# Kernel tuning notes

Measured on AMD Instinct MI355X. Metric: run time of the kernel, lower is better.

Reference implementation:

```python
import jax, jax.numpy as jnp
import numpy as np

NUM_HEAD = 8
HEAD_DIM = 64
MAX_LEN = 2048
FEAT_DIM = 512
BATCH = 2
TEMPERATURE = 10000.0


def positional_encoding(L, F, temperature=TEMPERATURE):
    # Faithful port of get_positional_encoding (torch.range is inclusive -> L / F elements)
    embed = jnp.arange(L, dtype=jnp.float32)
    dim_t = jnp.arange(F, dtype=jnp.float32)
    dim_t = temperature ** (2.0 * jnp.floor(dim_t / 2.0) / F)
    pos = embed[:, None] / dim_t                      # (L, F)
    pos = jnp.stack([jnp.sin(pos[:, 0::2]), jnp.cos(pos[:, 1::2])], axis=2)  # (L, F//2, 2)
    return pos.reshape(1, L, F)


def setup_inputs() -> dict:
    key = jax.random.key(0)
    ks = jax.random.split(key, 7)
    D = NUM_HEAD * HEAD_DIM
    scale = 1.0 / np.sqrt(FEAT_DIM)
    return {
        "inputs": jax.random.normal(ks[0], (BATCH, FEAT_DIM, MAX_LEN), dtype=jnp.float32),
        "Wq": jax.random.normal(ks[1], (D, FEAT_DIM), dtype=jnp.float32) * scale,
        "bq": jax.random.normal(ks[2], (D,), dtype=jnp.float32) * 0.01,
        "Wk": jax.random.normal(ks[3], (D, FEAT_DIM), dtype=jnp.float32) * scale,
        "bk": jax.random.normal(ks[4], (D,), dtype=jnp.float32) * 0.01,
        "Wv": jax.random.normal(ks[5], (D, FEAT_DIM), dtype=jnp.float32) * scale,
        "bv": jax.random.normal(ks[6], (D,), dtype=jnp.float32) * 0.01,
    }


def reference(inputs, Wq, bq, Wk, bk, Wv, bv):
    B, F, L = inputs.shape
    H, d = NUM_HEAD, HEAD_DIM
    pos = positional_encoding(L, F)                   # (1, L, F)
    x = jnp.transpose(inputs, (0, 2, 1))              # (B, L, F)
    qk_in = x + pos
    q = (qk_in @ Wq.T + bq).reshape(B, L, H, d)       # (B, L, H, d)
    k = (qk_in @ Wk.T + bk).reshape(B, L, H, d)
    v = x @ Wv.T + bv                                 # computed but unused (bug in original)
    del v
    # NOTE: original uses KEY heads as values (multi_head_value built from key)
    scores = jnp.einsum("bqhd,bkhd->bhqk", q, k) * (float(d) ** -0.5)
    attn = jax.nn.softmax(scores, axis=-1)            # (B, H, L, L)
    dist = jnp.einsum("bhqk,bkhd->bqhd", attn, k).reshape(B, L, H * d)
    attn_out = jnp.transpose(attn, (0, 2, 3, 1))      # (B, L, L, H) == cat of head splits on -1
    return dist, attn_out
```

## Files before the change

kernel.cpp:

```cpp
#include <hip/hip_runtime.h>
#include <math.h>

constexpr int LSEQ = 2048;
constexpr int FEAT = 512;
constexpr int NH = 8;
constexpr int DM = 512;
constexpr int NB = 2;

typedef __bf16 bf16x8 __attribute__((ext_vector_type(8)));
typedef unsigned short u16x8 __attribute__((ext_vector_type(8)));
typedef unsigned int u32x4 __attribute__((ext_vector_type(4)));
typedef float f32x4 __attribute__((ext_vector_type(4)));

#define EXPC 0.18033688011112042f

__device__ inline f32x4 mfma16(u16x8 a, u16x8 b, f32x4 c) {
  return __builtin_amdgcn_mfma_f32_16x16x32_bf16(
      __builtin_bit_cast(bf16x8, a), __builtin_bit_cast(bf16x8, b), c, 0, 0, 0);
}
__device__ inline unsigned cvtpk(float lo, float hi) {
  unsigned r;
  asm("v_cvt_pk_bf16_f32 %0, %1, %2" : "=v"(r) : "v"(lo), "v"(hi));
  return r;
}
__device__ inline u16x8 ldbf8(const unsigned short* p) {
  return *reinterpret_cast<const u16x8*>(p);
}

__global__ __launch_bounds__(256) void pos_kernel(float* __restrict__ posT) {
  int idx = blockIdx.x * 256 + threadIdx.x;
  int l = idx & (LSEQ - 1);
  int f = idx >> 11;
  int i = f >> 1;
  double t = exp((double)i * (9.210340371976184 / 256.0));
  float ang = (float)((double)l / t);
  posT[idx] = (f & 1) ? cosf(ang) : sinf(ang);
}

__global__ __launch_bounds__(256) void prep_kernel(const float* __restrict__ x,
                                                   const float* __restrict__ posT,
                                                   unsigned short* __restrict__ abuf) {
  __shared__ float As[64 * 68];
  const int t = threadIdx.x;
  const int bid = blockIdx.x;
  const int ft = bid & 7, lt = (bid >> 3) & 31, b = bid >> 8;
  const int f0 = ft * 64, l0 = lt * 64;
#pragma unroll
  for (int rep = 0; rep < 4; ++rep) {
    int fl = rep * 16 + (t >> 4), l4 = (t & 15) * 4;
    float4 xv = *(const float4*)(x + ((size_t)b * FEAT + f0 + fl) * LSEQ + l0 + l4);
    float4 pv = *(const float4*)(posT + (size_t)(f0 + fl) * LSEQ + l0 + l4);
    *(float4*)&As[fl * 68 + l4] = make_float4(xv.x + pv.x, xv.y + pv.y, xv.z + pv.z, xv.w + pv.w);
  }
  __syncthreads();
  const int ll = t >> 2, fc = t & 3;
#pragma unroll
  for (int rep = 0; rep < 4; ++rep) {
    int fb = (fc + rep * 4) * 4;
    float v0 = As[(fb + 0) * 68 + ll];
    float v1 = As[(fb + 1) * 68 + ll];
    float v2 = As[(fb + 2) * 68 + ll];
    float v3 = As[(fb + 3) * 68 + ll];
    uint2 u = make_uint2(cvtpk(v0, v1), cvtpk(v2, v3));
    *(uint2*)(abuf + ((size_t)(b * LSEQ + l0 + ll)) * 512 + f0 + fb) = u;
  }
}

__global__ __launch_bounds__(256) void wcvt_kernel(const float* __restrict__ Wq,
                                                   const float* __restrict__ Wk,
                                                   unsigned short* __restrict__ wbuf) {
  int i8 = blockIdx.x * 256 + threadIdx.x;
  size_t base = (size_t)i8 * 8;
  const float* src = (base < (size_t)512 * 512) ? Wq + base : Wk + (base - (size_t)512 * 512);
  float4 a = *(const float4*)src;
  float4 b4 = *(const float4*)(src + 4);
  *(uint2*)(wbuf + base) = make_uint2(cvtpk(a.x, a.y), cvtpk(a.z, a.w));
  *(uint2*)(wbuf + base + 4) = make_uint2(cvtpk(b4.x, b4.y), cvtpk(b4.z, b4.w));
}

__global__ __launch_bounds__(256) void proj_kernel(
    const unsigned short* __restrict__ abuf, const unsigned short* __restrict__ wbuf,
    const float* __restrict__ bq, const float* __restrict__ bk,
    unsigned short* __restrict__ qb, unsigned short* __restrict__ kb,
    unsigned short* __restrict__ kT) {
  const int t = threadIdx.x;
  const int c0 = blockIdx.x * 64;
  const int r0 = blockIdx.y * 64;
  const int w = t >> 6, l = t & 63;
  const int lr = l & 15, g = l >> 4;
  const int c0w = c0 + (w >> 1) * 32;
  const int r0w = r0 + (w & 1) * 32;
  f32x4 acc[2][2];
#pragma unroll
  for (int i = 0; i < 2; ++i)
#pragma unroll
    for (int j = 0; j < 2; ++j) acc[i][j] = (f32x4){0.f, 0.f, 0.f, 0.f};
  for (int f0 = 0; f0 < FEAT; f0 += 32) {
    u16x8 a0 = ldbf8(wbuf + (size_t)(c0w + lr) * 512 + f0 + g * 8);
    u16x8 a1 = ldbf8(wbuf + (size_t)(c0w + 16 + lr) * 512 + f0 + g * 8);
    u16x8 b0 = ldbf8(abuf + (size_t)(r0w + lr) * 512 + f0 + g * 8);
    u16x8 b1 = ldbf8(abuf + (size_t)(r0w + 16 + lr) * 512 + f0 + g * 8);
    acc[0][0] = mfma16(a0, b0, acc[0][0]);
    acc[0][1] = mfma16(a0, b1, acc[0][1]);
    acc[1][0] = mfma16(a1, b0, acc[1][0]);
    acc[1][1] = mfma16(a1, b1, acc[1][1]);
  }
  const int isK = (c0 >= DM);
  const float* bias = isK ? bk : bq;
  unsigned short* ob = isK ? kb : qb;
  const int cb = c0w & (DM - 1);
#pragma unroll
  for (int ch = 0; ch < 2; ++ch) {
    int c = cb + ch * 16 + g * 4;
    float b0v = bias[c], b1v = bias[c + 1], b2v = bias[c + 2], b3v = bias[c + 3];
#pragma unroll
    for (int rh = 0; rh < 2; ++rh) {
      int r = r0w + rh * 16 + lr;
      f32x4 v = acc[ch][rh];
      uint2 u = make_uint2(cvtpk(v[0] + b0v, v[1] + b1v), cvtpk(v[2] + b2v, v[3] + b3v));
      *(uint2*)(ob + (size_t)r * 512 + c) = u;
      if (isK) {
        int bsel = r >> 11, lq = r & (LSEQ - 1);
        unsigned short* kp = kT + ((size_t)(bsel * 512 + c)) * 2048 + lq;
        kp[0] = (unsigned short)(u.x & 0xffff);
        kp[2048] = (unsigned short)(u.x >> 16);
        kp[2 * 2048] = (unsigned short)(u.y & 0xffff);
        kp[3 * 2048] = (unsigned short)(u.y >> 16);
      }
    }
  }
}

__global__ __launch_bounds__(512) void pass1_kernel(
    const unsigned short* __restrict__ qb, const unsigned short* __restrict__ kb,
    float* __restrict__ lpart) {
  const int t = threadIdx.x;
  const int bid = blockIdx.x;
  const int sp = bid & 7, qt = (bid >> 3) & 31, b = bid >> 8;
  const int q0 = qt * 64;
  const int h = t >> 6, l = t & 63;
  const int lr = l & 15, g = l >> 4;
  u16x8 qf[4][2];
#pragma unroll
  for (int Mt = 0; Mt < 4; ++Mt)
#pragma unroll
    for (int dh = 0; dh < 2; ++dh)
      qf[Mt][dh] = ldbf8(qb + (size_t)(b * LSEQ + q0 + Mt * 16 + lr) * 512 + h * 64 + dh * 32 + g * 8);
  float sum[4] = {0.f, 0.f, 0.f, 0.f};
  for (int slab = 0; slab < 8; ++slab) {
    const int kk0 = sp * 256 + slab * 32;
    u16x8 af[2][2];
#pragma unroll
    for (int kh = 0; kh < 2; ++kh)
#pragma unroll
      for (int dh = 0; dh < 2; ++dh)
        af[kh][dh] = ldbf8(kb + (size_t)(b * LSEQ + kk0 + kh * 16 + lr) * 512 + h * 64 + dh * 32 + g * 8);
#pragma unroll
    for (int Mt = 0; Mt < 4; ++Mt)
#pragma unroll
      for (int kh = 0; kh < 2; ++kh) {
        f32x4 s = (f32x4){0.f, 0.f, 0.f, 0.f};
        s = mfma16(af[kh][0], qf[Mt][0], s);
        s = mfma16(af[kh][1], qf[Mt][1], s);
        sum[Mt] += exp2f(s[0] * EXPC) + exp2f(s[1] * EXPC) +
                   exp2f(s[2] * EXPC) + exp2f(s[3] * EXPC);
      }
  }
#pragma unroll
  for (int Mt = 0; Mt < 4; ++Mt) {
    float v = sum[Mt];
    v += __shfl_xor(v, 16);
    v += __shfl_xor(v, 32);
    if ((l & 48) == 0)
      lpart[((size_t)((b * 8 + sp) * LSEQ) + q0 + Mt * 16 + lr) * 8 + h] = v;
  }
}

__global__ __launch_bounds__(512) void pass2_kernel(
    const unsigned short* __restrict__ qb, const unsigned short* __restrict__ kb,
    const unsigned short* __restrict__ kT, const float* __restrict__ lpart,
    float* __restrict__ attn, float* __restrict__ dist, float* __restrict__ distp) {
  __shared__ float Ps[2 * 32 * 292];
  __shared__ float linv[256];
  const int t = threadIdx.x;
  const int bid = blockIdx.x;
  const int qt = bid & 63;
  const int sp = (bid >> 6) & 1;
  const int b = bid >> 7;
  const int q0 = qt * 32;
  if (t < 256) {
    int q = t >> 3, hh = t & 7;
    float s = 0.f;
#pragma unroll
    for (int p = 0; p < 8; ++p)
      s += lpart[((size_t)((b * 8 + p) * LSEQ) + q0 + q) * 8 + hh];
    linv[t] = 1.0f / s;
  }
  __syncthreads();
  const int h = t >> 6, l = t & 63;
  const int lr = l & 15, g = l >> 4;
  u16x8 qf[2][2];
#pragma unroll
  for (int Mt = 0; Mt < 2; ++Mt)
#pragma unroll
    for (int dh = 0; dh < 2; ++dh)
      qf[Mt][dh] = ldbf8(qb + (size_t)(b * LSEQ + q0 + Mt * 16 + lr) * 512 + h * 64 + dh * 32 + g * 8);
  float lv[2] = {linv[lr * 8 + h], linv[(16 + lr) * 8 + h]};
  f32x4 dacc[2][4];
#pragma unroll
  for (int Mt = 0; Mt < 2; ++Mt)
#pragma unroll
    for (int Nd = 0; Nd < 4; ++Nd) dacc[Mt][Nd] = (f32x4){0.f, 0.f, 0.f, 0.f};

  const int kkb = sp * 1024;
  for (int slab = 0; slab < 32; ++slab) {
    const int kk0 = kkb + slab * 32;
    float* Pc = &Ps[(slab & 1) * 9344];
    u16x8 af[2][2];
#pragma unroll
    for (int kh = 0; kh < 2; ++kh)
#pragma unroll
      for (int dh = 0; dh < 2; ++dh)
        af[kh][dh] = ldbf8(kb + (size_t)(b * LSEQ + kk0 + kh * 16 + lr) * 512 + h * 64 + dh * 32 + g * 8);
    u16x8 bt[4];
#pragma unroll
    for (int Nd = 0; Nd < 4; ++Nd)
      bt[Nd] = ldbf8(kT + (size_t)(b * 512 + h * 64 + Nd * 16 + lr) * 2048 + kk0 + g * 8);
#pragma unroll
    for (int Mt = 0; Mt < 2; ++Mt)
#pragma unroll
      for (int kh = 0; kh < 2; ++kh) {
        f32x4 s = (f32x4){0.f, 0.f, 0.f, 0.f};
        s = mfma16(af[kh][0], qf[Mt][0], s);
        s = mfma16(af[kh][1], qf[Mt][1], s);
        f32x4 e = {exp2f(s[0] * EXPC) * lv[Mt], exp2f(s[1] * EXPC) * lv[Mt],
                   exp2f(s[2] * EXPC) * lv[Mt], exp2f(s[3] * EXPC) * lv[Mt]};
        *(f32x4*)&Pc[(Mt * 16 + lr) * 292 + h * 36 + kh * 16 + g * 4] = e;
      }
    __syncthreads();
#pragma unroll
    for (int rep = 0; rep < 4; ++rep) {
      int F = rep * 512 + t;
      int q = F >> 6, kk = (F >> 1) & 31, hh = (F & 1) * 4;
      int pb = q * 292 + hh * 36 + kk;
      f32x4 v = {Pc[pb], Pc[pb + 36], Pc[pb + 72], Pc[pb + 108]};
      __builtin_nontemporal_store(v,
          (f32x4*)(attn + ((size_t)(b * LSEQ + q0 + q)) * (LSEQ * NH) + (size_t)(kk0 + kk) * 8 + hh));
    }
#pragma unroll
    for (int Mt = 0; Mt < 2; ++Mt) {
      int pb = (Mt * 16 + lr) * 292 + h * 36 + g * 8;
      f32x4 plo = *(const f32x4*)&Pc[pb];
      f32x4 phi = *(const f32x4*)&Pc[pb + 4];
      u32x4 pu = {cvtpk(plo[0], plo[1]), cvtpk(plo[2], plo[3]),
                  cvtpk(phi[0], phi[1]), cvtpk(phi[2], phi[3])};
      u16x8 pa = __builtin_bit_cast(u16x8, pu);
#pragma unroll
      for (int Nd = 0; Nd < 4; ++Nd)
        dacc[Mt][Nd] = mfma16(pa, bt[Nd], dacc[Mt][Nd]);
    }
  }
  float* dp = sp ? distp : dist;
#pragma unroll
  for (int Mt = 0; Mt < 2; ++Mt)
#pragma unroll
    for (int Nd = 0; Nd < 4; ++Nd)
#pragma unroll
      for (int r = 0; r < 4; ++r)
        dp[((size_t)(b * LSEQ + q0 + Mt * 16 + g * 4 + r)) * 512 + h * 64 + Nd * 16 + lr] =
            dacc[Mt][Nd][r];
}

__global__ __launch_bounds__(256) void combine_kernel(const float* __restrict__ p,
                                                      float* __restrict__ dist) {
  int i4 = blockIdx.x * 256 + threadIdx.x;
  const float4* p4 = (const float4*)p;
  float4 a = ((float4*)dist)[i4], c = p4[i4];
  ((float4*)dist)[i4] = make_float4(a.x + c.x, a.y + c.y, a.z + c.z, a.w + c.w);
}

extern "C" void kernel_launch(void* const* d_in, const int* in_sizes, int n_in,
                              void* d_out, int out_size, void* d_ws, size_t ws_size,
                              hipStream_t stream) {
  const float* x  = (const float*)d_in[0];
  const float* Wq = (const float*)d_in[1];
  const float* bq = (const float*)d_in[2];
  const float* Wk = (const float*)d_in[3];
  const float* bk = (const float*)d_in[4];
  float* out  = (float*)d_out;
  float* dist = out;
  float* attn = out + (size_t)NB * LSEQ * DM;
  float* ws = (float*)d_ws;
  float* posT  = ws;
  unsigned short* abuf = (unsigned short*)(ws + 1048576);
  unsigned short* wbuf = (unsigned short*)(ws + 2097152);
  unsigned short* qb   = (unsigned short*)(ws + 2359296);
  unsigned short* kb   = (unsigned short*)(ws + 3407872);
  unsigned short* kT   = (unsigned short*)(ws + 4456448);
  float* lpart = ws + 5505024;
  float* distp = ws;

  pos_kernel<<<4096, 256, 0, stream>>>(posT);
  prep_kernel<<<512, 256, 0, stream>>>(x, posT, abuf);
  wcvt_kernel<<<256, 256, 0, stream>>>(Wq, Wk, wbuf);
  proj_kernel<<<dim3(16, 64), 256, 0, stream>>>(abuf, wbuf, bq, bk, qb, kb, kT);
  pass1_kernel<<<512, 512, 0, stream>>>(qb, kb, lpart);
  pass2_kernel<<<256, 512, 0, stream>>>(qb, kb, kT, lpart, attn, dist, distp);
  combine_kernel<<<2048, 256, 0, stream>>>(distp, dist);
}
```

Before: 171.1 us.

## Fuse softmax passes into one kernel, compute positional encoding inline, fold scale into Q

After: 223.6 us. +30.7%, slower.

```diff
diff --git a/kernel.cpp b/kernel.cpp
--- a/kernel.cpp
+++ b/kernel.cpp
@@ -13,6 +13,7 @@
 typedef float f32x4 __attribute__((ext_vector_type(4)));
 
 #define EXPC 0.18033688011112042f
+#define L2TEN4 13.287712379549449f
 
 __device__ inline f32x4 mfma16(u16x8 a, u16x8 b, f32x4 c) {
   return __builtin_amdgcn_mfma_f32_16x16x32_bf16(
@@ -26,31 +27,47 @@
 __device__ inline u16x8 ldbf8(const unsigned short* p) {
   return *reinterpret_cast<const u16x8*>(p);
 }
-
-__global__ __launch_bounds__(256) void pos_kernel(float* __restrict__ posT) {
-  int idx = blockIdx.x * 256 + threadIdx.x;
-  int l = idx & (LSEQ - 1);
-  int f = idx >> 11;
-  int i = f >> 1;
-  double t = exp((double)i * (9.210340371976184 / 256.0));
-  float ang = (float)((double)l / t);
-  posT[idx] = (f & 1) ? cosf(ang) : sinf(ang);
-}
-
-__global__ __launch_bounds__(256) void prep_kernel(const float* __restrict__ x,
-                                                   const float* __restrict__ posT,
-                                                   unsigned short* __restrict__ abuf) {
+__device__ inline f32x4 qk_chain(u16x8 a0, u16x8 a1, u16x8 q0, u16x8 q1) {
+  f32x4 s = (f32x4){0.f, 0.f, 0.f, 0.f};
+  s = mfma16(a0, q0, s);
+  s = mfma16(a1, q1, s);
+  return s;
+}
+
+__global__ __launch_bounds__(256) void prep_all_kernel(
+    const float* __restrict__ x, const float* __restrict__ Wq,
+    const float* __restrict__ Wk, unsigned short* __restrict__ abuf,
+    unsigned short* __restrict__ wbuf) {
+  const int t = threadIdx.x;
+  const int bid0 = blockIdx.x;
+  if (bid0 >= 512) {
+    int i8 = (bid0 - 512) * 256 + t;
+    size_t base = (size_t)i8 * 8;
+    const float* src = (base < (size_t)512 * 512) ? Wq + base : Wk + (base - (size_t)512 * 512);
+    float4 a = *(const float4*)src;
+    float4 b4 = *(const float4*)(src + 4);
+    *(uint2*)(wbuf + base) = make_uint2(cvtpk(a.x, a.y), cvtpk(a.z, a.w));
+    *(uint2*)(wbuf + base + 4) = make_uint2(cvtpk(b4.x, b4.y), cvtpk(b4.z, b4.w));
+    return;
+  }
   __shared__ float As[64 * 68];
-  const int t = threadIdx.x;
-  const int bid = blockIdx.x;
-  const int ft = bid & 7, lt = (bid >> 3) & 31, b = bid >> 8;
+  const int ft = bid0 & 7, lt = (bid0 >> 3) & 31, b = bid0 >> 8;
   const int f0 = ft * 64, l0 = lt * 64;
 #pragma unroll
   for (int rep = 0; rep < 4; ++rep) {
     int fl = rep * 16 + (t >> 4), l4 = (t & 15) * 4;
-    float4 xv = *(const float4*)(x + ((size_t)b * FEAT + f0 + fl) * LSEQ + l0 + l4);
-    float4 pv = *(const float4*)(posT + (size_t)(f0 + fl) * LSEQ + l0 + l4);
-    *(float4*)&As[fl * 68 + l4] = make_float4(xv.x + pv.x, xv.y + pv.y, xv.z + pv.z, xv.w + pv.w);
+    int f = f0 + fl;
+    float invt = exp2f((float)(f >> 1) * (-L2TEN4 / 256.0f));
+    float4 xv = *(const float4*)(x + ((size_t)b * FEAT + f) * LSEQ + l0 + l4);
+    float a0 = (float)(l0 + l4 + 0) * invt;
+    float a1 = (float)(l0 + l4 + 1) * invt;
+    float a2 = (float)(l0 + l4 + 2) * invt;
+    float a3 = (float)(l0 + l4 + 3) * invt;
+    float4 pv;
+    if (f & 1) { pv.x = cosf(a0); pv.y = cosf(a1); pv.z = cosf(a2); pv.w = cosf(a3); }
+    else       { pv.x = sinf(a0); pv.y = sinf(a1); pv.z = sinf(a2); pv.w = sinf(a3); }
+    *(float4*)&As[fl * 68 + l4] =
+        make_float4(xv.x + pv.x, xv.y + pv.y, xv.z + pv.z, xv.w + pv.w);
   }
   __syncthreads();
   const int ll = t >> 2, fc = t & 3;
@@ -61,21 +78,9 @@
     float v1 = As[(fb + 1) * 68 + ll];
     float v2 = As[(fb + 2) * 68 + ll];
     float v3 = As[(fb + 3) * 68 + ll];
-    uint2 u = make_uint2(cvtpk(v0, v1), cvtpk(v2, v3));
-    *(uint2*)(abuf + ((size_t)(b * LSEQ + l0 + ll)) * 512 + f0 + fb) = u;
-  }
-}
-
-__global__ __launch_bounds__(256) void wcvt_kernel(const float* __restrict__ Wq,
-                                                   const float* __restrict__ Wk,
-                                                   unsigned short* __restrict__ wbuf) {
-  int i8 = blockIdx.x * 256 + threadIdx.x;
-  size_t base = (size_t)i8 * 8;
-  const float* src = (base < (size_t)512 * 512) ? Wq + base : Wk + (base - (size_t)512 * 512);
-  float4 a = *(const float4*)src;
-  float4 b4 = *(const float4*)(src + 4);
-  *(uint2*)(wbuf + base) = make_uint2(cvtpk(a.x, a.y), cvtpk(a.z, a.w));
-  *(uint2*)(wbuf + base + 4) = make_uint2(cvtpk(b4.x, b4.y), cvtpk(b4.z, b4.w));
+    *(uint2*)(abuf + ((size_t)(b * LSEQ + l0 + ll)) * 512 + f0 + fb) =
+        make_uint2(cvtpk(v0, v1), cvtpk(v2, v3));
+  }
 }
 
 __global__ __launch_bounds__(256) void proj_kernel(
@@ -108,6 +113,7 @@
   const int isK = (c0 >= DM);
   const float* bias = isK ? bk : bq;
   unsigned short* ob = isK ? kb : qb;
+  const float scale = isK ? 1.0f : EXPC;
   const int cb = c0w & (DM - 1);
 #pragma unroll
   for (int ch = 0; ch < 2; ++ch) {
@@ -117,7 +123,8 @@
     for (int rh = 0; rh < 2; ++rh) {
       int r = r0w + rh * 16 + lr;
       f32x4 v = acc[ch][rh];
-      uint2 u = make_uint2(cvtpk(v[0] + b0v, v[1] + b1v), cvtpk(v[2] + b2v, v[3] + b3v));
+      uint2 u = make_uint2(cvtpk((v[0] + b0v) * scale, (v[1] + b1v) * scale),
+                           cvtpk((v[2] + b2v) * scale, (v[3] + b3v) * scale));
       *(uint2*)(ob + (size_t)r * 512 + c) = u;
       if (isK) {
         int bsel = r >> 11, lq = r & (LSEQ - 1);
@@ -131,115 +138,62 @@
   }
 }
 
-__global__ __launch_bounds__(512) void pass1_kernel(
+__global__ __launch_bounds__(512) void pass2_kernel(
     const unsigned short* __restrict__ qb, const unsigned short* __restrict__ kb,
-    float* __restrict__ lpart) {
+    const unsigned short* __restrict__ kT, float* __restrict__ attn,
+    float* __restrict__ dist) {
+  __shared__ float Ps[2 * 16 * 292];
   const int t = threadIdx.x;
   const int bid = blockIdx.x;
-  const int sp = bid & 7, qt = (bid >> 3) & 31, b = bid >> 8;
-  const int q0 = qt * 64;
+  const int qt = bid & 127;
+  const int b = bid >> 7;
+  const int q0 = qt * 16;
   const int h = t >> 6, l = t & 63;
   const int lr = l & 15, g = l >> 4;
-  u16x8 qf[4][2];
-#pragma unroll
-  for (int Mt = 0; Mt < 4; ++Mt)
-#pragma unroll
-    for (int dh = 0; dh < 2; ++dh)
-      qf[Mt][dh] = ldbf8(qb + (size_t)(b * LSEQ + q0 + Mt * 16 + lr) * 512 + h * 64 + dh * 32 + g * 8);
-  float sum[4] = {0.f, 0.f, 0.f, 0.f};
-  for (int slab = 0; slab < 8; ++slab) {
-    const int kk0 = sp * 256 + slab * 32;
-    u16x8 af[2][2];
-#pragma unroll
-    for (int kh = 0; kh < 2; ++kh)
-#pragma unroll
-      for (int dh = 0; dh < 2; ++dh)
-        af[kh][dh] = ldbf8(kb + (size_t)(b * LSEQ + kk0 + kh * 16 + lr) * 512 + h * 64 + dh * 32 + g * 8);
-#pragma unroll
-    for (int Mt = 0; Mt < 4; ++Mt)
-#pragma unroll
-      for (int kh = 0; kh < 2; ++kh) {
-        f32x4 s = (f32x4){0.f, 0.f, 0.f, 0.f};
-        s = mfma16(af[kh][0], qf[Mt][0], s);
-        s = mfma16(af[kh][1], qf[Mt][1], s);
-        sum[Mt] += exp2f(s[0] * EXPC) + exp2f(s[1] * EXPC) +
-                   exp2f(s[2] * EXPC) + exp2f(s[3] * EXPC);
-      }
-  }
-#pragma unroll
-  for (int Mt = 0; Mt < 4; ++Mt) {
-    float v = sum[Mt];
-    v += __shfl_xor(v, 16);
-    v += __shfl_xor(v, 32);
-    if ((l & 48) == 0)
-      lpart[((size_t)((b * 8 + sp) * LSEQ) + q0 + Mt * 16 + lr) * 8 + h] = v;
-  }
-}
-
-__global__ __launch_bounds__(512) void pass2_kernel(
-    const unsigned short* __restrict__ qb, const unsigned short* __restrict__ kb,
-    const unsigned short* __restrict__ kT, const float* __restrict__ lpart,
-    float* __restrict__ attn, float* __restrict__ dist, float* __restrict__ distp) {
-  __shared__ float Ps[2 * 32 * 292];
-  __shared__ float linv[256];
-  const int t = threadIdx.x;
-  const int bid = blockIdx.x;
-  const int qt = bid & 63;
-  const int sp = (bid >> 6) & 1;
-  const int b = bid >> 7;
-  const int q0 = qt * 32;
-  if (t < 256) {
-    int q = t >> 3, hh = t & 7;
-    float s = 0.f;
-#pragma unroll
-    for (int p = 0; p < 8; ++p)
-      s += lpart[((size_t)((b * 8 + p) * LSEQ) + q0 + q) * 8 + hh];
-    linv[t] = 1.0f / s;
-  }
-  __syncthreads();
-  const int h = t >> 6, l = t & 63;
-  const int lr = l & 15, g = l >> 4;
-  u16x8 qf[2][2];
-#pragma unroll
-  for (int Mt = 0; Mt < 2; ++Mt)
-#pragma unroll
-    for (int dh = 0; dh < 2; ++dh)
-      qf[Mt][dh] = ldbf8(qb + (size_t)(b * LSEQ + q0 + Mt * 16 + lr) * 512 + h * 64 + dh * 32 + g * 8);
-  float lv[2] = {linv[lr * 8 + h], linv[(16 + lr) * 8 + h]};
-  f32x4 dacc[2][4];
-#pragma unroll
-  for (int Mt = 0; Mt < 2; ++Mt)
-#pragma unroll
-    for (int Nd = 0; Nd < 4; ++Nd) dacc[Mt][Nd] = (f32x4){0.f, 0.f, 0.f, 0.f};
-
-  const int kkb = sp * 1024;
-  for (int slab = 0; slab < 32; ++slab) {
-    const int kk0 = kkb + slab * 32;
-    float* Pc = &Ps[(slab & 1) * 9344];
-    u16x8 af[2][2];
-#pragma unroll
-    for (int kh = 0; kh < 2; ++kh)
-#pragma unroll
-      for (int dh = 0; dh < 2; ++dh)
-        af[kh][dh] = ldbf8(kb + (size_t)(b * LSEQ + kk0 + kh * 16 + lr) * 512 + h * 64 + dh * 32 + g * 8);
+  u16x8 qf[2];
+#pragma unroll
+  for (int dh = 0; dh < 2; ++dh)
+    qf[dh] = ldbf8(qb + (size_t)(b * LSEQ + q0 + lr) * 512 + h * 64 + dh * 32 + g * 8);
+
+  float sum = 0.f;
+  for (int slab = 0; slab < 64; ++slab) {
+    const int kk0 = slab * 32;
+#pragma unroll
+    for (int kh = 0; kh < 2; ++kh) {
+      const unsigned short* kp = kb + (size_t)(b * LSEQ + kk0 + kh * 16 + lr) * 512 + h * 64 + g * 8;
+      u16x8 a0 = ldbf8(kp);
+      u16x8 a1 = ldbf8(kp + 32);
+      f32x4 s = qk_chain(a0, a1, qf[0], qf[1]);
+      sum += exp2f(s[0]) + exp2f(s[1]) + exp2f(s[2]) + exp2f(s[3]);
+    }
+  }
+  sum += __shfl_xor(sum, 16);
+  sum += __shfl_xor(sum, 32);
+  const float linv = 1.0f / sum;
+
+  f32x4 dacc[4];
+#pragma unroll
+  for (int Nd = 0; Nd < 4; ++Nd) dacc[Nd] = (f32x4){0.f, 0.f, 0.f, 0.f};
+  for (int slab = 0; slab < 64; ++slab) {
+    const int kk0 = slab * 32;
+    float* Pc = &Ps[(slab & 1) * 4672];
     u16x8 bt[4];
 #pragma unroll
     for (int Nd = 0; Nd < 4; ++Nd)
       bt[Nd] = ldbf8(kT + (size_t)(b * 512 + h * 64 + Nd * 16 + lr) * 2048 + kk0 + g * 8);
 #pragma unroll
-    for (int Mt = 0; Mt < 2; ++Mt)
-#pragma unroll
-      for (int kh = 0; kh < 2; ++kh) {
-        f32x4 s = (f32x4){0.f, 0.f, 0.f, 0.f};
-        s = mfma16(af[kh][0], qf[Mt][0], s);
-        s = mfma16(af[kh][1], qf[Mt][1], s);
-        f32x4 e = {exp2f(s[0] * EXPC) * lv[Mt], exp2f(s[1] * EXPC) * lv[Mt],
-                   exp2f(s[2] * EXPC) * lv[Mt], exp2f(s[3] * EXPC) * lv[Mt]};
-        *(f32x4*)&Pc[(Mt * 16 + lr) * 292 + h * 36 + kh * 16 + g * 4] = e;
-      }
+    for (int kh = 0; kh < 2; ++kh) {
+      const unsigned short* kp = kb + (size_t)(b * LSEQ + kk0 + kh * 16 + lr) * 512 + h * 64 + g * 8;
+      u16x8 a0 = ldbf8(kp);
+      u16x8 a1 = ldbf8(kp + 32);
+      f32x4 s = qk_chain(a0, a1, qf[0], qf[1]);
+      f32x4 e = {exp2f(s[0]) * linv, exp2f(s[1]) * linv,
+                 exp2f(s[2]) * linv, exp2f(s[3]) * linv};
+      *(f32x4*)&Pc[lr * 292 + h * 36 + kh * 16 + g * 4] = e;
+    }
     __syncthreads();
 #pragma unroll
-    for (int rep = 0; rep < 4; ++rep) {
+    for (int rep = 0; rep < 2; ++rep) {
       int F = rep * 512 + t;
       int q = F >> 6, kk = (F >> 1) & 31, hh = (F & 1) * 4;
       int pb = q * 292 + hh * 36 + kk;
@@ -247,9 +201,8 @@
       __builtin_nontemporal_store(v,
           (f32x4*)(attn + ((size_t)(b * LSEQ + q0 + q)) * (LSEQ * NH) + (size_t)(kk0 + kk) * 8 + hh));
     }
-#pragma unroll
-    for (int Mt = 0; Mt < 2; ++Mt) {
-      int pb = (Mt * 16 + lr) * 292 + h * 36 + g * 8;
+    {
+      int pb = lr * 292 + h * 36 + g * 8;
       f32x4 plo = *(const f32x4*)&Pc[pb];
       f32x4 phi = *(const f32x4*)&Pc[pb + 4];
       u32x4 pu = {cvtpk(plo[0], plo[1]), cvtpk(plo[2], plo[3]),
@@ -257,26 +210,14 @@
       u16x8 pa = __builtin_bit_cast(u16x8, pu);
 #pragma unroll
       for (int Nd = 0; Nd < 4; ++Nd)
-        dacc[Mt][Nd] = mfma16(pa, bt[Nd], dacc[Mt][Nd]);
-    }
-  }
-  float* dp = sp ? distp : dist;
-#pragma unroll
-  for (int Mt = 0; Mt < 2; ++Mt)
-#pragma unroll
-    for (int Nd = 0; Nd < 4; ++Nd)
-#pragma unroll
-      for (int r = 0; r < 4; ++r)
-        dp[((size_t)(b * LSEQ + q0 + Mt * 16 + g * 4 + r)) * 512 + h * 64 + Nd * 16 + lr] =
-            dacc[Mt][Nd][r];
-}
-
-__global__ __launch_bounds__(256) void combine_kernel(const float* __restrict__ p,
-                                                      float* __restrict__ dist) {
-  int i4 = blockIdx.x * 256 + threadIdx.x;
-  const float4* p4 = (const float4*)p;
-  float4 a = ((float4*)dist)[i4], c = p4[i4];
-  ((float4*)dist)[i4] = make_float4(a.x + c.x, a.y + c.y, a.z + c.z, a.w + c.w);
+        dacc[Nd] = mfma16(pa, bt[Nd], dacc[Nd]);
+    }
+  }
+#pragma unroll
+  for (int Nd = 0; Nd < 4; ++Nd)
+#pragma unroll
+    for (int r = 0; r < 4; ++r)
+      dist[((size_t)(b * LSEQ + q0 + g * 4 + r)) * 512 + h * 64 + Nd * 16 + lr] = dacc[Nd][r];
 }
 
 extern "C" void kernel_launch(void* const* d_in, const int* in_sizes, int n_in,
@@ -291,20 +232,13 @@
   float* dist = out;
   float* attn = out + (size_t)NB * LSEQ * DM;
   float* ws = (float*)d_ws;
-  float* posT  = ws;
-  unsigned short* abuf = (unsigned short*)(ws + 1048576);
-  unsigned short* wbuf = (unsigned short*)(ws + 2097152);
-  unsigned short* qb   = (unsigned short*)(ws + 2359296);
-  unsigned short* kb   = (unsigned short*)(ws + 3407872);
-  unsigned short* kT   = (unsigned short*)(ws + 4456448);
-  float* lpart = ws + 5505024;
-  float* distp = ws;
-
-  pos_kernel<<<4096, 256, 0, stream>>>(posT);
-  prep_kernel<<<512, 256, 0, stream>>>(x, posT, abuf);
-  wcvt_kernel<<<256, 256, 0, stream>>>(Wq, Wk, wbuf);
+  unsigned short* abuf = (unsigned short*)(ws);
+  unsigned short* wbuf = (unsigned short*)(ws + 1048576);
+  unsigned short* qb   = (unsigned short*)(ws + 1310720);
+  unsigned short* kb   = (unsigned short*)(ws + 2359296);
+  unsigned short* kT   = (unsigned short*)(ws + 3407872);
+
+  prep_all_kernel<<<768, 256, 0, stream>>>(x, Wq, Wk, abuf, wbuf);
   proj_kernel<<<dim3(16, 64), 256, 0, stream>>>(abuf, wbuf, bq, bk, qb, kb, kT);
-  pass1_kernel<<<512, 512, 0, stream>>>(qb, kb, lpart);
-  pass2_kernel<<<256, 512, 0, stream>>>(qb, kb, kT, lpart, attn, dist, distp);
-  combine_kernel<<<2048, 256, 0, stream>>>(distp, dist);
-}
+  pass2_kernel<<<256, 512, 0, stream>>>(qb, kb, kT, attn, dist);
+}
```

## Fuse positional encoding and weight conversion into one prep kernel, prescale Q

Applied to the files above, without the earlier changes.

Measured after the change: 162.1 us. -5.3%, faster.

```diff
diff --git a/kernel.cpp b/kernel.cpp
--- a/kernel.cpp
+++ b/kernel.cpp
@@ -13,6 +13,7 @@
 typedef float f32x4 __attribute__((ext_vector_type(4)));
 
 #define EXPC 0.18033688011112042f
+#define L2TEN4 13.287712379549449f
 
 __device__ inline f32x4 mfma16(u16x8 a, u16x8 b, f32x4 c) {
   return __builtin_amdgcn_mfma_f32_16x16x32_bf16(
@@ -26,31 +27,47 @@
 __device__ inline u16x8 ldbf8(const unsigned short* p) {
   return *reinterpret_cast<const u16x8*>(p);
 }
-
-__global__ __launch_bounds__(256) void pos_kernel(float* __restrict__ posT) {
-  int idx = blockIdx.x * 256 + threadIdx.x;
-  int l = idx & (LSEQ - 1);
-  int f = idx >> 11;
-  int i = f >> 1;
-  double t = exp((double)i * (9.210340371976184 / 256.0));
-  float ang = (float)((double)l / t);
-  posT[idx] = (f & 1) ? cosf(ang) : sinf(ang);
-}
-
-__global__ __launch_bounds__(256) void prep_kernel(const float* __restrict__ x,
-                                                   const float* __restrict__ posT,
-                                                   unsigned short* __restrict__ abuf) {
+__device__ inline f32x4 qk_chain(u16x8 a0, u16x8 a1, u16x8 q0, u16x8 q1) {
+  f32x4 s = (f32x4){0.f, 0.f, 0.f, 0.f};
+  s = mfma16(a0, q0, s);
+  s = mfma16(a1, q1, s);
+  return s;
+}
+
+__global__ __launch_bounds__(256) void prep_all_kernel(
+    const float* __restrict__ x, const float* __restrict__ Wq,
+    const float* __restrict__ Wk, unsigned short* __restrict__ abuf,
+    unsigned short* __restrict__ wbuf) {
+  const int t = threadIdx.x;
+  const int bid0 = blockIdx.x;
+  if (bid0 >= 512) {
+    int i8 = (bid0 - 512) * 256 + t;
+    size_t base = (size_t)i8 * 8;
+    const float* src = (base < (size_t)512 * 512) ? Wq + base : Wk + (base - (size_t)512 * 512);
+    float4 a = *(const float4*)src;
+    float4 b4 = *(const float4*)(src + 4);
+    *(uint2*)(wbuf + base) = make_uint2(cvtpk(a.x, a.y), cvtpk(a.z, a.w));
+    *(uint2*)(wbuf + base + 4) = make_uint2(cvtpk(b4.x, b4.y), cvtpk(b4.z, b4.w));
+    return;
+  }
   __shared__ float As[64 * 68];
-  const int t = threadIdx.x;
-  const int bid = blockIdx.x;
-  const int ft = bid & 7, lt = (bid >> 3) & 31, b = bid >> 8;
+  const int ft = bid0 & 7, lt = (bid0 >> 3) & 31, b = bid0 >> 8;
   const int f0 = ft * 64, l0 = lt * 64;
 #pragma unroll
   for (int rep = 0; rep < 4; ++rep) {
     int fl = rep * 16 + (t >> 4), l4 = (t & 15) * 4;
-    float4 xv = *(const float4*)(x + ((size_t)b * FEAT + f0 + fl) * LSEQ + l0 + l4);
-    float4 pv = *(const float4*)(posT + (size_t)(f0 + fl) * LSEQ + l0 + l4);
-    *(float4*)&As[fl * 68 + l4] = make_float4(xv.x + pv.x, xv.y + pv.y, xv.z + pv.z, xv.w + pv.w);
+    int f = f0 + fl;
+    float invt = exp2f((float)(f >> 1) * (-L2TEN4 / 256.0f));
+    float4 xv = *(const float4*)(x + ((size_t)b * FEAT + f) * LSEQ + l0 + l4);
+    float a0 = (float)(l0 + l4 + 0) * invt;
+    float a1 = (float)(l0 + l4 + 1) * invt;
+    float a2 = (float)(l0 + l4 + 2) * invt;
+    float a3 = (float)(l0 + l4 + 3) * invt;
+    float4 pv;
+    if (f & 1) { pv.x = cosf(a0); pv.y = cosf(a1); pv.z = cosf(a2); pv.w = cosf(a3); }
+    else       { pv.x = sinf(a0); pv.y = sinf(a1); pv.z = sinf(a2); pv.w = sinf(a3); }
+    *(float4*)&As[fl * 68 + l4] =
+        make_float4(xv.x + pv.x, xv.y + pv.y, xv.z + pv.z, xv.w + pv.w);
   }
   __syncthreads();
   const int ll = t >> 2, fc = t & 3;
@@ -61,21 +78,9 @@
     float v1 = As[(fb + 1) * 68 + ll];
     float v2 = As[(fb + 2) * 68 + ll];
     float v3 = As[(fb + 3) * 68 + ll];
-    uint2 u = make_uint2(cvtpk(v0, v1), cvtpk(v2, v3));
-    *(uint2*)(abuf + ((size_t)(b * LSEQ + l0 + ll)) * 512 + f0 + fb) = u;
-  }
-}
-
-__global__ __launch_bounds__(256) void wcvt_kernel(const float* __restrict__ Wq,
-                                                   const float* __restrict__ Wk,
-                                                   unsigned short* __restrict__ wbuf) {
-  int i8 = blockIdx.x * 256 + threadIdx.x;
-  size_t base = (size_t)i8 * 8;
-  const float* src = (base < (size_t)512 * 512) ? Wq + base : Wk + (base - (size_t)512 * 512);
-  float4 a = *(const float4*)src;
-  float4 b4 = *(const float4*)(src + 4);
-  *(uint2*)(wbuf + base) = make_uint2(cvtpk(a.x, a.y), cvtpk(a.z, a.w));
-  *(uint2*)(wbuf + base + 4) = make_uint2(cvtpk(b4.x, b4.y), cvtpk(b4.z, b4.w));
+    *(uint2*)(abuf + ((size_t)(b * LSEQ + l0 + ll)) * 512 + f0 + fb) =
+        make_uint2(cvtpk(v0, v1), cvtpk(v2, v3));
+  }
 }
 
 __global__ __launch_bounds__(256) void proj_kernel(
@@ -108,6 +113,7 @@
   const int isK = (c0 >= DM);
   const float* bias = isK ? bk : bq;
   unsigned short* ob = isK ? kb : qb;
+  const float scale = isK ? 1.0f : EXPC;
   const int cb = c0w & (DM - 1);
 #pragma unroll
   for (int ch = 0; ch < 2; ++ch) {
@@ -117,7 +123,8 @@
     for (int rh = 0; rh < 2; ++rh) {
       int r = r0w + rh * 16 + lr;
       f32x4 v = acc[ch][rh];
-      uint2 u = make_uint2(cvtpk(v[0] + b0v, v[1] + b1v), cvtpk(v[2] + b2v, v[3] + b3v));
+      uint2 u = make_uint2(cvtpk((v[0] + b0v) * scale, (v[1] + b1v) * scale),
+                           cvtpk((v[2] + b2v) * scale, (v[3] + b3v) * scale));
       *(uint2*)(ob + (size_t)r * 512 + c) = u;
       if (isK) {
         int bsel = r >> 11, lq = r & (LSEQ - 1);
@@ -159,11 +166,8 @@
     for (int Mt = 0; Mt < 4; ++Mt)
 #pragma unroll
       for (int kh = 0; kh < 2; ++kh) {
-        f32x4 s = (f32x4){0.f, 0.f, 0.f, 0.f};
-        s = mfma16(af[kh][0], qf[Mt][0], s);
-        s = mfma16(af[kh][1], qf[Mt][1], s);
-        sum[Mt] += exp2f(s[0] * EXPC) + exp2f(s[1] * EXPC) +
-                   exp2f(s[2] * EXPC) + exp2f(s[3] * EXPC);
+        f32x4 s = qk_chain(af[kh][0], af[kh][1], qf[Mt][0], qf[Mt][1]);
+        sum[Mt] += exp2f(s[0]) + exp2f(s[1]) + exp2f(s[2]) + exp2f(s[3]);
       }
   }
 #pragma unroll
@@ -184,9 +188,9 @@
   __shared__ float linv[256];
   const int t = threadIdx.x;
   const int bid = blockIdx.x;
-  const int qt = bid & 63;
-  const int sp = (bid >> 6) & 1;
-  const int b = bid >> 7;
+  const int qt = bid >> 2;
+  const int b = (bid >> 1) & 1;
+  const int sp = bid & 1;
   const int q0 = qt * 32;
   if (t < 256) {
     int q = t >> 3, hh = t & 7;
@@ -230,11 +234,9 @@
     for (int Mt = 0; Mt < 2; ++Mt)
 #pragma unroll
       for (int kh = 0; kh < 2; ++kh) {
-        f32x4 s = (f32x4){0.f, 0.f, 0.f, 0.f};
-        s = mfma16(af[kh][0], qf[Mt][0], s);
-        s = mfma16(af[kh][1], qf[Mt][1], s);
-        f32x4 e = {exp2f(s[0] * EXPC) * lv[Mt], exp2f(s[1] * EXPC) * lv[Mt],
-                   exp2f(s[2] * EXPC) * lv[Mt], exp2f(s[3] * EXPC) * lv[Mt]};
+        f32x4 s = qk_chain(af[kh][0], af[kh][1], qf[Mt][0], qf[Mt][1]);
+        f32x4 e = {exp2f(s[0]) * lv[Mt], exp2f(s[1]) * lv[Mt],
+                   exp2f(s[2]) * lv[Mt], exp2f(s[3]) * lv[Mt]};
         *(f32x4*)&Pc[(Mt * 16 + lr) * 292 + h * 36 + kh * 16 + g * 4] = e;
       }
     __syncthreads();
@@ -291,18 +293,15 @@
   float* dist = out;
   float* attn = out + (size_t)NB * LSEQ * DM;
   float* ws = (float*)d_ws;
-  float* posT  = ws;
-  unsigned short* abuf = (unsigned short*)(ws + 1048576);
-  unsigned short* wbuf = (unsigned short*)(ws + 2097152);
-  unsigned short* qb   = (unsigned short*)(ws + 2359296);
-  unsigned short* kb   = (unsigned short*)(ws + 3407872);
-  unsigned short* kT   = (unsigned short*)(ws + 4456448);
-  float* lpart = ws + 5505024;
+  unsigned short* abuf = (unsigned short*)(ws);
+  unsigned short* wbuf = (unsigned short*)(ws + 1048576);
+  unsigned short* qb   = (unsigned short*)(ws + 2097152);
+  unsigned short* kb   = (unsigned short*)(ws + 3145728);
+  unsigned short* kT   = (unsigned short*)(ws + 4194304);
+  float* lpart = ws + 5242880;
   float* distp = ws;
 
-  pos_kernel<<<4096, 256, 0, stream>>>(posT);
-  prep_kernel<<<512, 256, 0, stream>>>(x, posT, abuf);
-  wcvt_kernel<<<256, 256, 0, stream>>>(Wq, Wk, wbuf);
+  prep_all_kernel<<<768, 256, 0, stream>>>(x, Wq, Wk, abuf, wbuf);
   proj_kernel<<<dim3(16, 64), 256, 0, stream>>>(abuf, wbuf, bq, bk, qb, kb, kT);
   pass1_kernel<<<512, 512, 0, stream>>>(qb, kb, lpart);
   pass2_kernel<<<256, 512, 0, stream>>>(qb, kb, kT, lpart, attn, dist, distp);
```
